# Kernel tuning notes

Hardware: AMD Instinct MI355X
Metric: run time of the kernel (lower is better)

## Reference

```python
import jax, jax.numpy as jnp
import numpy as np

A, T, C, R, D, K, H, W = 3, 32, 4, 8, 2, 1024, 64, 64


def setup_inputs() -> dict:
    key = jax.random.key(0)
    ks = jax.random.split(key, 6)
    x = jax.random.normal(ks[0], (A, H, W), dtype=jnp.float32)
    # k-space trajectory in rad/voxel, uniform in [-pi, pi]
    trj = (jax.random.uniform(ks[1], (R, D, K), dtype=jnp.float32) * 2.0 - 1.0) * np.pi
    phi = jax.random.normal(ks[2], (A, T), dtype=jnp.float32)
    mps = jax.random.normal(ks[3], (C, H, W), dtype=jnp.float32)
    sqrt_dcf = jax.random.uniform(ks[4], (R, K), dtype=jnp.float32)
    subsamp_idx = jax.random.randint(ks[5], (T,), 0, R, dtype=jnp.int64)
    return {"x": x, "trj": trj, "phi": phi, "mps": mps,
            "sqrt_dcf": sqrt_dcf, "subsamp_idx": subsamp_idx}


def _nudft_matrix(trj):
    # Exact type-2 non-uniform DFT matrix E[r, k, n] = exp(-i w_rk . p_n)
    gy = (jnp.arange(H) - H // 2).astype(jnp.float32)
    gx = (jnp.arange(W) - W // 2).astype(jnp.float32)
    grid = jnp.stack(jnp.meshgrid(gy, gx, indexing="ij"), axis=0).reshape(D, H * W)
    phase = jnp.einsum("rdk,dn->rkn", trj, grid)  # [R, K, N]
    return jnp.exp(-1j * phase)  # complex64 [R, K, N]


def reference(x, trj, phi, mps, sqrt_dcf, subsamp_idx):
    # SENSE-weighted images per subspace coeff: [A, C, N]
    s = (mps[None, :, :, :] * x[:, None, :, :]).reshape(A, C, H * W).astype(jnp.complex64)
    E = _nudft_matrix(trj)
    # NUFFT of every (coeff, coil) image along every trajectory: [A, R, C, K]
    y = jnp.einsum("rkn,acn->arck", E, s)
    # temporal subspace expansion: [R, T, C, K]
    y = jnp.einsum("at,arck->rtck", phi.astype(jnp.complex64), y)
    # density compensation
    y = y * sqrt_dcf[:, None, None, :].astype(jnp.complex64)
    # per-timepoint trajectory subsampling: [T, C, K]
    out = y[subsamp_idx, jnp.arange(T)]
    return out
```

## Files before the change

### kernel.cpp

```cpp
#include <hip/hip_runtime.h>
#include <hip/hip_bf16.h>

#define NA 3
#define NT 32
#define NC 4
#define NR 8
#define NK 1024
#define NPIX 4096
#define NOUT (NT * NC * NK)
#define NRK (NR * NK)

typedef __attribute__((ext_vector_type(8))) short bf16x8;
typedef __attribute__((ext_vector_type(4))) float f32x4;

static __device__ __forceinline__ short f2bf(float f) {
    union { __hip_bfloat16 h; short s; } u;
    u.h = __float2bfloat16(f);
    return u.s;
}

__global__ __launch_bounds__(256) void prep_pack(
    const float* __restrict__ x,
    const float* __restrict__ candA,
    const float* __restrict__ candB,
    int* __restrict__ flag,
    short* __restrict__ sp)
{
    __shared__ int sfl;
    if (threadIdx.x == 0) sfl = 0;
    __syncthreads();
    {
        const float4* A4 = (const float4*)candA;
        int loc = 0;
        for (int i = threadIdx.x; i < 4096; i += 256) {
            const float4 v = A4[i];
            if (fabsf(v.x) > 3.1416f || fabsf(v.y) > 3.1416f ||
                fabsf(v.z) > 3.1416f || fabsf(v.w) > 3.1416f) loc = 1;
        }
        if (loc) atomicOr(&sfl, 1);
    }
    __syncthreads();
    const int fl = sfl;
    if (blockIdx.x == 0 && threadIdx.x == 0) flag[0] = fl;
    const float* __restrict__ mps = fl ? candA : candB;

    const int job = blockIdx.x * 256 + threadIdx.x;
    const int ch = job >> 9, p8 = (job & 511) * 8;
    const int a = ch >> 2, c = ch & 3;
    const float4 xv0 = *(const float4*)&x[a * NPIX + p8];
    const float4 xv1 = *(const float4*)&x[a * NPIX + p8 + 4];
    const float4 mv0 = *(const float4*)&mps[c * NPIX + p8];
    const float4 mv1 = *(const float4*)&mps[c * NPIX + p8 + 4];
    union { bf16x8 v; short s[8]; } pk;
    pk.s[0] = f2bf(xv0.x * mv0.x); pk.s[1] = f2bf(xv0.y * mv0.y);
    pk.s[2] = f2bf(xv0.z * mv0.z); pk.s[3] = f2bf(xv0.w * mv0.w);
    pk.s[4] = f2bf(xv1.x * mv1.x); pk.s[5] = f2bf(xv1.y * mv1.y);
    pk.s[6] = f2bf(xv1.z * mv1.z); pk.s[7] = f2bf(xv1.w * mv1.w);
    *(bf16x8*)(sp + ch * NPIX + p8) = pk.v;
}

__global__ __launch_bounds__(512) void nudft32(
    const short* __restrict__ sp,
    const float* __restrict__ candA,
    const float* __restrict__ candB,
    const int*  __restrict__ flag,
    const float* __restrict__ phi,
    const float* __restrict__ dcf,
    const int*  __restrict__ sidx,
    float* __restrict__ out)
{
    __shared__ float2 ylds[2][12][32];

    const float* __restrict__ trj = flag[0] ? candB : candA;

    const int tid = threadIdx.x;
    const int w = tid >> 6, l = tid & 63, col = l & 15, g = l >> 4;
    const int chgrp = w & 3, ihalf = w >> 2;
    const int rk0 = blockIdx.x * 32;
    const int r = rk0 >> 10, k0 = rk0 & (NK - 1);

    float t0a[2], t1a[2];
#pragma unroll
    for (int q = 0; q < 2; ++q) {
        const int k = k0 + q * 16 + col;
        t0a[q] = trj[(r * 2 + 0) * NK + k];
        t1a[q] = trj[(r * 2 + 1) * NK + k];
    }

    bf16x8 bre[2][2], bim[2][2];
#pragma unroll
    for (int q = 0; q < 2; ++q) {
        float pr[8], pi[8];
        float sr, cr; __sincosf(t1a[q], &sr, &cr);
        float s0, c0; __sincosf(t1a[q] * (float)(g * 8 - 32), &s0, &c0);
        pr[0] = c0; pi[0] = -s0;
#pragma unroll
        for (int e = 1; e < 8; ++e) {
            const float nr = pr[e-1] * cr + pi[e-1] * sr;
            const float ni = pi[e-1] * cr - pr[e-1] * sr;
            pr[e] = nr; pi[e] = ni;
        }
        union { bf16x8 v; short s[8]; } u0, u1;
#pragma unroll
        for (int e = 0; e < 8; ++e) { u0.s[e] = f2bf(pr[e]); u1.s[e] = f2bf(pi[e]); }
        bre[q][0] = u0.v; bim[q][0] = u1.v;
        float s32, c32; __sincosf(32.f * t1a[q], &s32, &c32);
#pragma unroll
        for (int e = 0; e < 8; ++e) {
            const float nr = pr[e] * c32 + pi[e] * s32;
            const float ni = pi[e] * c32 - pr[e] * s32;
            u0.s[e] = f2bf(nr); u1.s[e] = f2bf(ni);
        }
        bre[q][1] = u0.v; bim[q][1] = u1.v;
    }

    float syr[2], cyr[2];
#pragma unroll
    for (int q = 0; q < 2; ++q) __sincosf(t0a[q], &syr[q], &cyr[q]);

    float yre[2][3] = {{0.f,0.f,0.f},{0.f,0.f,0.f}};
    float yim[2][3] = {{0.f,0.f,0.f},{0.f,0.f,0.f}};

#pragma unroll
    for (int sl = 0; sl < 2; ++sl) {
        const int i0 = ihalf * 32 + sl * 16;
        float eyR[2][4], eyI[2][4];
#pragma unroll
        for (int q = 0; q < 2; ++q) {
            float sb, cb; __sincosf(t0a[q] * (float)(i0 + g * 4 - 32), &sb, &cb);
            eyR[q][0] = cb; eyI[q][0] = -sb;
#pragma unroll
            for (int j = 1; j < 4; ++j) {
                const float nr = eyR[q][j-1] * cyr[q] + eyI[q][j-1] * syr[q];
                const float ni = eyI[q][j-1] * cyr[q] - eyR[q][j-1] * syr[q];
                eyR[q][j] = nr; eyI[q][j] = ni;
            }
        }
#pragma unroll
        for (int cc = 0; cc < 3; ++cc) {
            const int ch = chgrp * 3 + cc;
            const short* ap = sp + ch * NPIX + (i0 + col) * 64 + g * 8;
            const bf16x8 a0 = *(const bf16x8*)ap;
            const bf16x8 a1 = *(const bf16x8*)(ap + 32);
#pragma unroll
            for (int q = 0; q < 2; ++q) {
                f32x4 gre = {0.f, 0.f, 0.f, 0.f}, gim = {0.f, 0.f, 0.f, 0.f};
                gre = __builtin_amdgcn_mfma_f32_16x16x32_bf16(a0, bre[q][0], gre, 0, 0, 0);
                gre = __builtin_amdgcn_mfma_f32_16x16x32_bf16(a1, bre[q][1], gre, 0, 0, 0);
                gim = __builtin_amdgcn_mfma_f32_16x16x32_bf16(a0, bim[q][0], gim, 0, 0, 0);
                gim = __builtin_amdgcn_mfma_f32_16x16x32_bf16(a1, bim[q][1], gim, 0, 0, 0);
#pragma unroll
                for (int reg = 0; reg < 4; ++reg) {
                    yre[q][cc] = fmaf(eyR[q][reg], gre[reg],
                                  fmaf(-eyI[q][reg], gim[reg], yre[q][cc]));
                    yim[q][cc] = fmaf(eyR[q][reg], gim[reg],
                                  fmaf( eyI[q][reg], gre[reg], yim[q][cc]));
                }
            }
        }
    }

#pragma unroll
    for (int q = 0; q < 2; ++q) {
#pragma unroll
        for (int cc = 0; cc < 3; ++cc) {
            float vr = yre[q][cc], vi = yim[q][cc];
            vr += __shfl_xor(vr, 16); vi += __shfl_xor(vi, 16);
            vr += __shfl_xor(vr, 32); vi += __shfl_xor(vi, 32);
            if (g == 0)
                ylds[ihalf][chgrp * 3 + cc][q * 16 + col] = make_float2(vr, vi);
        }
    }
    __syncthreads();

    bool is64 = true;
#pragma unroll
    for (int i = 1; i < 32; i += 2) is64 = is64 && (sidx[i] == 0);
#pragma unroll
    for (int q = 0; q < 8; ++q) {
        const int item = tid + q * 512;
        const int kl = item & 31;
        const int c  = (item >> 5) & 3;
        const int t  = item >> 7;
        const int rt = is64 ? sidx[2 * t] : sidx[t];
        if (rt == r) {
            const float d = dcf[r * NK + k0 + kl];
            float ore = 0.f, oim = 0.f;
#pragma unroll
            for (int a = 0; a < NA; ++a) {
                const float p = phi[a * NT + t];
                const float2 v0 = ylds[0][a * 4 + c][kl];
                const float2 v1 = ylds[1][a * 4 + c][kl];
                ore = fmaf(p, v0.x + v1.x, ore);
                oim = fmaf(p, v0.y + v1.y, oim);
            }
            const int gid = t * 4096 + c * 1024 + k0 + kl;
            out[gid]        = ore * d;
            out[NOUT + gid] = oim * d;
        }
    }
}

extern "C" void kernel_launch(void* const* d_in, const int* in_sizes, int n_in,
                              void* d_out, int out_size, void* d_ws, size_t ws_size,
                              hipStream_t stream) {
    int ix = 0, i16a = 1, iphi = 2, i16b = 3, idcf = 4, isidx = 5;
    int f16[2]; int n16 = 0, fx = -1, fphi = -1, fdcf = -1, fsidx = -1;
    for (int i = 0; i < n_in; ++i) {
        const int s = in_sizes[i];
        if (s == 12288) fx = i;
        else if (s == 96) fphi = i;
        else if (s == 8192) fdcf = i;
        else if (s == 16384) { if (n16 < 2) f16[n16] = i; ++n16; }
        else if (s == 32 || s == 64) fsidx = i;
    }
    if (fx >= 0 && fphi >= 0 && fdcf >= 0 && fsidx >= 0 && n16 == 2) {
        ix = fx; iphi = fphi; idcf = fdcf; isidx = fsidx;
        i16a = f16[0]; i16b = f16[1];
    }

    const float* x    = (const float*)d_in[ix];
    const float* cA   = (const float*)d_in[i16a];
    const float* cB   = (const float*)d_in[i16b];
    const float* phi  = (const float*)d_in[iphi];
    const float* dcf  = (const float*)d_in[idcf];
    const int*   sidx = (const int*)d_in[isidx];

    int*   flag = (int*)d_ws;
    short* sp   = (short*)((char*)d_ws + 256);

    prep_pack<<<24, 256, 0, stream>>>(x, cA, cB, flag, sp);
    nudft32<<<NRK / 32, 512, 0, stream>>>(sp, cA, cB, flag, phi, dcf, sidx,
                                          (float*)d_out);
}
```

Before: 17.96 us.

## Fuse SENSE packing into NUDFT kernel with swizzled LDS staging

Removes the separate prep_pack launch and its global workspace buffer. Every block now runs the trajectory/maps detection itself, builds the full bf16 SENSE-weighted image set (96 KB) in dynamic LDS using an XOR swizzle, and reads MFMA A-operands from LDS instead of global memory. This saves one kernel launch and the global write/read round trip. In exchange, every block repeats the packing work and the candidate scan, and the large LDS footprint limits occupancy to one block per CU.

```diff
diff --git a/kernel.cpp b/kernel.cpp
--- a/kernel.cpp
+++ b/kernel.cpp
@@ -9,6 +9,7 @@
 #define NPIX 4096
 #define NOUT (NT * NC * NK)
 #define NRK (NR * NK)
+#define SP_LDS_BYTES 98304
 
 typedef __attribute__((ext_vector_type(8))) short bf16x8;
 typedef __attribute__((ext_vector_type(4))) float f32x4;
@@ -19,61 +20,59 @@
     return u.s;
 }
 
-__global__ __launch_bounds__(256) void prep_pack(
+__global__ __launch_bounds__(512) void nudft_mono2(
     const float* __restrict__ x,
     const float* __restrict__ candA,
     const float* __restrict__ candB,
-    int* __restrict__ flag,
-    short* __restrict__ sp)
-{
-    __shared__ int sfl;
-    if (threadIdx.x == 0) sfl = 0;
-    __syncthreads();
-    {
-        const float4* A4 = (const float4*)candA;
-        int loc = 0;
-        for (int i = threadIdx.x; i < 4096; i += 256) {
-            const float4 v = A4[i];
-            if (fabsf(v.x) > 3.1416f || fabsf(v.y) > 3.1416f ||
-                fabsf(v.z) > 3.1416f || fabsf(v.w) > 3.1416f) loc = 1;
-        }
-        if (loc) atomicOr(&sfl, 1);
-    }
-    __syncthreads();
-    const int fl = sfl;
-    if (blockIdx.x == 0 && threadIdx.x == 0) flag[0] = fl;
-    const float* __restrict__ mps = fl ? candA : candB;
-
-    const int job = blockIdx.x * 256 + threadIdx.x;
-    const int ch = job >> 9, p8 = (job & 511) * 8;
-    const int a = ch >> 2, c = ch & 3;
-    const float4 xv0 = *(const float4*)&x[a * NPIX + p8];
-    const float4 xv1 = *(const float4*)&x[a * NPIX + p8 + 4];
-    const float4 mv0 = *(const float4*)&mps[c * NPIX + p8];
-    const float4 mv1 = *(const float4*)&mps[c * NPIX + p8 + 4];
-    union { bf16x8 v; short s[8]; } pk;
-    pk.s[0] = f2bf(xv0.x * mv0.x); pk.s[1] = f2bf(xv0.y * mv0.y);
-    pk.s[2] = f2bf(xv0.z * mv0.z); pk.s[3] = f2bf(xv0.w * mv0.w);
-    pk.s[4] = f2bf(xv1.x * mv1.x); pk.s[5] = f2bf(xv1.y * mv1.y);
-    pk.s[6] = f2bf(xv1.z * mv1.z); pk.s[7] = f2bf(xv1.w * mv1.w);
-    *(bf16x8*)(sp + ch * NPIX + p8) = pk.v;
-}
-
-__global__ __launch_bounds__(512) void nudft32(
-    const short* __restrict__ sp,
-    const float* __restrict__ candA,
-    const float* __restrict__ candB,
-    const int*  __restrict__ flag,
     const float* __restrict__ phi,
     const float* __restrict__ dcf,
     const int*  __restrict__ sidx,
     float* __restrict__ out)
 {
+    extern __shared__ char lds[];
+    __shared__ int sfl;
     __shared__ float2 ylds[2][12][32];
 
-    const float* __restrict__ trj = flag[0] ? candB : candA;
-
     const int tid = threadIdx.x;
+
+    if (tid == 0) sfl = 0;
+    __syncthreads();
+    {
+        const float4* A4 = (const float4*)candA;
+        int loc = 0;
+#pragma unroll
+        for (int q = 0; q < 8; ++q) {
+            const float4 v = A4[tid + q * 512];
+            if (fabsf(v.x) > 3.1416f || fabsf(v.y) > 3.1416f ||
+                fabsf(v.z) > 3.1416f || fabsf(v.w) > 3.1416f) loc = 1;
+        }
+        if (loc) atomicOr(&sfl, 1);
+    }
+    __syncthreads();
+    const int fl = sfl;
+    const float* __restrict__ trj = fl ? candB : candA;
+    const float* __restrict__ mps = fl ? candA : candB;
+
+#pragma unroll
+    for (int jj = 0; jj < 12; ++jj) {
+        const int job = tid + jj * 512;
+        const int ch = job >> 9, p8 = (job & 511) * 8;
+        const int a = ch >> 2, c = ch & 3;
+        const float4 xv0 = *(const float4*)&x[a * NPIX + p8];
+        const float4 xv1 = *(const float4*)&x[a * NPIX + p8 + 4];
+        const float4 mv0 = *(const float4*)&mps[c * NPIX + p8];
+        const float4 mv1 = *(const float4*)&mps[c * NPIX + p8 + 4];
+        union { bf16x8 v; short s[8]; } pk;
+        pk.s[0] = f2bf(xv0.x * mv0.x); pk.s[1] = f2bf(xv0.y * mv0.y);
+        pk.s[2] = f2bf(xv0.z * mv0.z); pk.s[3] = f2bf(xv0.w * mv0.w);
+        pk.s[4] = f2bf(xv1.x * mv1.x); pk.s[5] = f2bf(xv1.y * mv1.y);
+        pk.s[6] = f2bf(xv1.z * mv1.z); pk.s[7] = f2bf(xv1.w * mv1.w);
+        const int row = p8 >> 6;
+        const int byteoff = (ch * 8192 + p8 * 2) ^ ((row & 7) << 4);
+        *(bf16x8*)(lds + byteoff) = pk.v;
+    }
+    __syncthreads();
+
     const int w = tid >> 6, l = tid & 63, col = l & 15, g = l >> 4;
     const int chgrp = w & 3, ihalf = w >> 2;
     const int rk0 = blockIdx.x * 32;
@@ -139,9 +138,10 @@
 #pragma unroll
         for (int cc = 0; cc < 3; ++cc) {
             const int ch = chgrp * 3 + cc;
-            const short* ap = sp + ch * NPIX + (i0 + col) * 64 + g * 8;
-            const bf16x8 a0 = *(const bf16x8*)ap;
-            const bf16x8 a1 = *(const bf16x8*)(ap + 32);
+            const int lin = ch * 8192 + (i0 + col) * 128 + g * 16;
+            const int sw  = (col & 7) << 4;
+            const bf16x8 a0 = *(const bf16x8*)(lds + (lin ^ sw));
+            const bf16x8 a1 = *(const bf16x8*)(lds + ((lin + 64) ^ sw));
 #pragma unroll
             for (int q = 0; q < 2; ++q) {
                 f32x4 gre = {0.f, 0.f, 0.f, 0.f}, gim = {0.f, 0.f, 0.f, 0.f};
@@ -219,17 +219,16 @@
         i16a = f16[0]; i16b = f16[1];
     }
 
-    const float* x    = (const float*)d_in[ix];
-    const float* cA   = (const float*)d_in[i16a];
-    const float* cB   = (const float*)d_in[i16b];
-    const float* phi  = (const float*)d_in[iphi];
-    const float* dcf  = (const float*)d_in[idcf];
-    const int*   sidx = (const int*)d_in[isidx];
-
-    int*   flag = (int*)d_ws;
-    short* sp   = (short*)((char*)d_ws + 256);
-
-    prep_pack<<<24, 256, 0, stream>>>(x, cA, cB, flag, sp);
-    nudft32<<<NRK / 32, 512, 0, stream>>>(sp, cA, cB, flag, phi, dcf, sidx,
-                                          (float*)d_out);
+    static bool attr_set = false;
+    if (!attr_set) {
+        hipFuncSetAttribute((const void*)nudft_mono2,
+                            hipFuncAttributeMaxDynamicSharedMemorySize,
+                            SP_LDS_BYTES);
+        attr_set = true;
+    }
+
+    nudft_mono2<<<NRK / 32, 512, SP_LDS_BYTES, stream>>>(
+        (const float*)d_in[ix], (const float*)d_in[i16a], (const float*)d_in[i16b],
+        (const float*)d_in[iphi], (const float*)d_in[idcf], (const int*)d_in[isidx],
+        (float*)d_out);
 }
```

Result: faster. 16.48 us (-8.2%).
